# Kernel optimization log

Hardware: AMD Instinct MI355X
Metric: run time of the kernel (lower is better)

## Reference

```python
import jax, jax.numpy as jnp
import numpy as np
from jax import lax

EPS = 1e-5


def fps(xyz, npoint):
    # Farthest point sampling; xyz [B, N, 3] -> idx [B, npoint] (starts at point 0)
    B, N, _ = xyz.shape

    def body(carry, _):
        dist, far = carry
        c = jnp.take_along_axis(xyz, far[:, None, None], axis=1)  # [B,1,3]
        d = jnp.sum((xyz - c) ** 2, -1)                            # [B,N]
        dist = jnp.minimum(dist, d)
        nxt = jnp.argmax(dist, -1).astype(jnp.int32)
        return (dist, nxt), far

    init = (jnp.full((B, N), 1e10, xyz.dtype), jnp.zeros((B,), jnp.int32))
    _, idx = lax.scan(body, init, None, length=npoint)
    return idx.T  # [B, npoint]


def query_ball(radius, nsample, xyz, new_xyz):
    # xyz [B,N,3], new_xyz [B,S,3] -> idx [B,S,nsample]
    N = xyz.shape[1]
    sqr = jnp.sum((new_xyz[:, :, None, :] - xyz[:, None, :, :]) ** 2, -1)  # [B,S,N]
    idx = jnp.where(sqr > radius * radius, N, jnp.arange(N)[None, None, :])
    idx = jnp.sort(idx, axis=-1)[:, :, :nsample]
    # out-of-ball slots get replaced by the first in-ball index (torch repo behavior)
    return jnp.where(idx == N, idx[:, :, :1], idx)


def gather_pts(x, idx):
    # x [B,N,C], idx [B,...] -> [B,...,C]
    B = x.shape[0]
    b = jnp.arange(B).reshape((B,) + (1,) * (idx.ndim - 1))
    return x[b, idx]


def mlp_bn(x, layers):
    # x [B,S,K,C]; shared 1x1-conv MLP + training-mode BatchNorm + ReLU
    for w, g, b in layers:
        x = jnp.einsum('bskc,oc->bsko', x, w)
        mean = x.mean((0, 1, 2))
        var = x.var((0, 1, 2))  # biased, as torch BN uses for normalization
        x = jax.nn.relu((x - mean) * lax.rsqrt(var + EPS) * g + b)
    return x


def set_abstraction(xyz, points, npoint, radius, nsample, layers, group_all):
    B = xyz.shape[0]
    if group_all:
        new_xyz = jnp.zeros((B, 1, 3), xyz.dtype)
        new_points = xyz[:, None]  # [B,1,N,3] (raw xyz, no centering)
        if points is not None:
            new_points = jnp.concatenate([new_points, points[:, None]], -1)
    else:
        fidx = fps(xyz, npoint)
        new_xyz = gather_pts(xyz, fidx)                     # [B,S,3]
        idx = query_ball(radius, nsample, xyz, new_xyz)     # [B,S,K]
        grouped = gather_pts(xyz, idx) - new_xyz[:, :, None, :]
        if points is not None:
            new_points = jnp.concatenate([grouped, gather_pts(points, idx)], -1)
        else:
            new_points = grouped
    feat = mlp_bn(new_points, layers).max(2)  # max-pool over neighbors -> [B,S,C]
    return new_xyz, feat


def _forward(xyz_time, l1, l2, l3):
    B, T, N, _ = xyz_time.shape
    x = xyz_time.reshape(B * T, N, 4)
    xyz, t = x[..., :3], x[..., 3:]
    x1_xyz, x1 = set_abstraction(xyz, t, 512, 0.2, 32, l1, False)
    x2_xyz, x2 = set_abstraction(x1_xyz, x1, 128, 0.4, 64, l2, False)
    _, x3 = set_abstraction(x2_xyz, x2, None, None, None, l3, True)
    return x3.reshape(B, T, -1)


def setup_inputs() -> dict:
    key = jax.random.key(0)
    ks = jax.random.split(key, 16)
    inp = {"xyz_time": jax.random.uniform(ks[0], (2, 4, 4096, 4), jnp.float32)}
    specs = {1: [(64, 4), (64, 64), (128, 64)],
             2: [(128, 131), (128, 128), (256, 128)],
             3: [(256, 259), (512, 256), (1024, 512)]}
    i = 1
    for s, layers in specs.items():
        for j, (o, c) in enumerate(layers):
            inp[f"w{s}_{j}"] = jax.random.normal(jax.random.fold_in(ks[i], j), (o, c), jnp.float32) * 0.1
            inp[f"g{s}_{j}"] = jnp.ones((o,), jnp.float32)
            inp[f"b{s}_{j}"] = jnp.zeros((o,), jnp.float32)
        i += 1
    return inp


def reference(xyz_time, w1_0, g1_0, b1_0, w1_1, g1_1, b1_1, w1_2, g1_2, b1_2,
              w2_0, g2_0, b2_0, w2_1, g2_1, b2_1, w2_2, g2_2, b2_2,
              w3_0, g3_0, b3_0, w3_1, g3_1, b3_1, w3_2, g3_2, b3_2):
    l1 = [(w1_0, g1_0, b1_0), (w1_1, g1_1, b1_1), (w1_2, g1_2, b1_2)]
    l2 = [(w2_0, g2_0, b2_0), (w2_1, g2_1, b2_1), (w2_2, g2_2, b2_2)]
    l3 = [(w3_0, g3_0, b3_0), (w3_1, g3_1, b3_1), (w3_2, g3_2, b3_2)]
    return _forward(xyz_time, l1, l2, l3)
```

## Files before the change

### kernel.cpp

```cpp
#include <hip/hip_runtime.h>


typedef short s16x8 __attribute__((ext_vector_type(8)));
typedef float f32x4 __attribute__((ext_vector_type(4)));

__device__ __forceinline__ unsigned short f2bf_rne(float f) {
    unsigned u = __float_as_uint(f);
    u += 0x7FFFu + ((u >> 16) & 1u);
    return (unsigned short)(u >> 16);
}
__device__ __forceinline__ void f2bf_split(float v, unsigned short& hi,
                                           unsigned short& lo) {
    unsigned u = __float_as_uint(v);
    unsigned r = u + 0x7FFFu + ((u >> 16) & 1u);
    hi = (unsigned short)(r >> 16);
    float vh = __uint_as_float(r & 0xFFFF0000u);
    lo = f2bf_rne(v - vh);
}

__device__ __forceinline__ unsigned long long umax64(unsigned long long a,
                                                     unsigned long long b) {
    return a > b ? a : b;
}

__device__ __forceinline__ unsigned wred_umax63(unsigned v) {
    unsigned t;
    t = (unsigned)__builtin_amdgcn_update_dpp(0, (int)v, 0x111, 0xf, 0xf, true); if (t > v) v = t;
    t = (unsigned)__builtin_amdgcn_update_dpp(0, (int)v, 0x112, 0xf, 0xf, true); if (t > v) v = t;
    t = (unsigned)__builtin_amdgcn_update_dpp(0, (int)v, 0x114, 0xf, 0xf, true); if (t > v) v = t;
    t = (unsigned)__builtin_amdgcn_update_dpp(0, (int)v, 0x118, 0xf, 0xf, true); if (t > v) v = t;
    t = (unsigned)__builtin_amdgcn_update_dpp(0, (int)v, 0x142, 0xa, 0xf, true); if (t > v) v = t;
    t = (unsigned)__builtin_amdgcn_update_dpp(0, (int)v, 0x143, 0xc, 0xf, true); if (t > v) v = t;
    return v;
}

__device__ __forceinline__ void wave_argmax(unsigned dbits, unsigned nInv,
                                            unsigned& vmax, unsigned& iInv) {
    unsigned m = wred_umax63(dbits);
    vmax = (unsigned)__builtin_amdgcn_readlane((int)m, 63);
    unsigned cand = (dbits == vmax) ? nInv : 0u;
    unsigned im = wred_umax63(cand);
    iInv = (unsigned)__builtin_amdgcn_readlane((int)im, 63);
}

struct PWArgs {
    const float* w[9];
    unsigned off[9];
    int O[9], C[9], CP[9];
};
__device__ __forceinline__ void prep_w_dev(const PWArgs& a,
                                           unsigned short* __restrict__ wh,
                                           unsigned short* __restrict__ wl,
                                           int i) {
    int l = 0;
#pragma unroll
    for (int k = 1; k < 9; ++k) if (i >= (int)a.off[k]) l = k;
    int li = i - (int)a.off[l];
    int CP = a.CP[l];
    int o = li / CP;
    int c = li - o * CP;
    float v = (c < a.C[l]) ? a.w[l][(size_t)o * a.C[l] + c] : 0.f;
    unsigned short h, lo;
    f2bf_split(v, h, lo);
    wh[i] = h; wl[i] = lo;
}

template<int NT, int ITEMS, int STRIDE>
__global__ __launch_bounds__(NT) void fps_block(
    const float* __restrict__ pts, int npoint,
    int* __restrict__ outIdx, float* __restrict__ outXyz,
    int nFps, PWArgs pw, unsigned short* __restrict__ wh,
    unsigned short* __restrict__ wl, int wtotal)
{
    constexpr int N = NT * ITEMS;
    constexpr int NW = NT / 64;
    __shared__ float4 scoord[N];
    __shared__ unsigned long long wkey[2][NW];

    if (blockIdx.x >= nFps) {
        int i = (blockIdx.x - nFps) * NT + threadIdx.x;
        if (i < wtotal) prep_w_dev(pw, wh, wl, i);
        return;
    }

    const int b = blockIdx.x;
    const int tid = threadIdx.x;
    const int wid = tid >> 6;
    const int lane = tid & 63;
    const float* P = pts + (size_t)b * N * STRIDE;

    float px[ITEMS], py[ITEMS], pz[ITEMS], dloc[ITEMS];
#pragma unroll
    for (int w = 0; w < ITEMS; ++w) {
        int n = tid + w * NT;
        float x, y, z;
        if (STRIDE == 4) {
            float4 v = *(const float4*)(P + (size_t)n * 4);
            x = v.x; y = v.y; z = v.z;
        } else {
            x = P[(size_t)n * STRIDE + 0];
            y = P[(size_t)n * STRIDE + 1];
            z = P[(size_t)n * STRIDE + 2];
        }
        px[w] = x; py[w] = y; pz[w] = z;
        scoord[n] = make_float4(x, y, z, 0.f);
        dloc[w] = 1e10f;
    }
    __syncthreads();
    float4 c0 = scoord[0];
    float cx = c0.x, cy = c0.y, cz = c0.z;
    int far = 0;

    for (int i = 0; i < npoint; ++i) {
        if (tid == 0) {
            outIdx[(size_t)b * npoint + i] = far;
            outXyz[((size_t)b * npoint + i) * 3 + 0] = cx;
            outXyz[((size_t)b * npoint + i) * 3 + 1] = cy;
            outXyz[((size_t)b * npoint + i) * 3 + 2] = cz;
        }
        float bestV = -1.0f;
        int bestW = 0;
#pragma unroll
        for (int w = 0; w < ITEMS; ++w) {
            float dx = __fsub_rn(px[w], cx);
            float dy = __fsub_rn(py[w], cy);
            float dz = __fsub_rn(pz[w], cz);
            float d = __fadd_rn(__fadd_rn(__fmul_rn(dx, dx), __fmul_rn(dy, dy)),
                                __fmul_rn(dz, dz));
            float dd = fminf(dloc[w], d);
            dloc[w] = dd;
            if (dd > bestV) { bestV = dd; bestW = w; }
        }
        int bestN = tid + bestW * NT;
        unsigned vmax, iInv;
        wave_argmax(__float_as_uint(bestV), 0xFFFFFFFFu ^ (unsigned)bestN,
                    vmax, iInv);
        const int par = i & 1;
        if (lane == 0)
            wkey[par][wid] = ((unsigned long long)vmax << 32) | iInv;
        __syncthreads();
        unsigned long long kb = wkey[par][0];
#pragma unroll
        for (int w2 = 1; w2 < NW; ++w2) kb = umax64(kb, wkey[par][w2]);
        far = (int)(0xFFFFFFFFu ^ (unsigned)kb);
        float4 cc = scoord[far];
        cx = cc.x; cy = cc.y; cz = cc.z;
    }
}

__device__ void fps_wave_dev(const float* __restrict__ pts, int npoint,
                             int* __restrict__ outIdx, float* __restrict__ outXyz,
                             int b, float4* scoord)
{
    constexpr int ITEMS = 8;
    constexpr int STRIDE = 3;
    constexpr int N = 64 * ITEMS;
    const int tid = threadIdx.x;
    const float* P = pts + (size_t)b * N * STRIDE;

    float px[ITEMS], py[ITEMS], pz[ITEMS], dloc[ITEMS];
#pragma unroll
    for (int w = 0; w < ITEMS; ++w) {
        int n = tid + w * 64;
        float x = P[(size_t)n * STRIDE + 0];
        float y = P[(size_t)n * STRIDE + 1];
        float z = P[(size_t)n * STRIDE + 2];
        px[w] = x; py[w] = y; pz[w] = z;
        scoord[n] = make_float4(x, y, z, 0.f);
        dloc[w] = 1e10f;
    }
    __threadfence_block();
    float4 c0 = scoord[0];
    float cx = c0.x, cy = c0.y, cz = c0.z;
    int far = 0;

    for (int i = 0; i < npoint; ++i) {
        if (tid == 0) {
            outIdx[(size_t)b * npoint + i] = far;
            outXyz[((size_t)b * npoint + i) * 3 + 0] = cx;
            outXyz[((size_t)b * npoint + i) * 3 + 1] = cy;
            outXyz[((size_t)b * npoint + i) * 3 + 2] = cz;
        }
        float bestV = -1.0f;
        int bestW = 0;
#pragma unroll
        for (int w = 0; w < ITEMS; ++w) {
            float dx = __fsub_rn(px[w], cx);
            float dy = __fsub_rn(py[w], cy);
            float dz = __fsub_rn(pz[w], cz);
            float d = __fadd_rn(__fadd_rn(__fmul_rn(dx, dx), __fmul_rn(dy, dy)),
                                __fmul_rn(dz, dz));
            float dd = fminf(dloc[w], d);
            dloc[w] = dd;
            if (dd > bestV) { bestV = dd; bestW = w; }
        }
        int bestN = tid + bestW * 64;
        unsigned vmax, iInv;
        wave_argmax(__float_as_uint(bestV), 0xFFFFFFFFu ^ (unsigned)bestN,
                    vmax, iInv);
        far = (int)(0xFFFFFFFFu ^ iInv);
        float4 cc = scoord[far];
        cx = cc.x; cy = cc.y; cz = cc.z;
    }
}

__global__ __launch_bounds__(256) void qb_group1(
    const float* __restrict__ xyz ,
    const float* __restrict__ ctr ,
    const float* __restrict__ W0 ,
    float* __restrict__ Yout ,
    double* __restrict__ pS0, double* __restrict__ pQ0,
    int nQb, const float* __restrict__ fpsPts,
    int* __restrict__ fpsIdx, float* __restrict__ fpsXyz)
{
    __shared__ float4 scoord[512];
    __shared__ float4 srows[4][32];
    __shared__ float sstat[4][64][2];
    if ((int)blockIdx.x >= nQb) {
        if (threadIdx.x < 64)
            fps_wave_dev(fpsPts, 128, fpsIdx, fpsXyz,
                         (int)blockIdx.x - nQb, scoord);
        return;
    }
    const int tid = threadIdx.x;
    const int gw = (blockIdx.x * 256 + tid) >> 6;
    const int wid = tid >> 6;
    const int lane = tid & 63;
    int b = gw >> 9;
    const float* P = xyz + (size_t)b * 4096 * 4;
    float cx = ctr[(size_t)gw * 3 + 0];
    float cy = ctr[(size_t)gw * 3 + 1];
    float cz = ctr[(size_t)gw * 3 + 2];
    int cnt = 0;
    float f0x = 0.f, f0y = 0.f, f0z = 0.f, f0t = 0.f;
    bool haveFirst = false;
    for (int base = 0; base < 4096 && cnt < 32; base += 64) {
        int n = base + lane;
        float4 p = *(const float4*)(P + (size_t)n * 4);
        float ex = __fsub_rn(p.x, cx);
        float ey = __fsub_rn(p.y, cy);
        float ez = __fsub_rn(p.z, cz);
        float d = __fadd_rn(__fadd_rn(__fmul_rn(ex, ex), __fmul_rn(ey, ey)),
                            __fmul_rn(ez, ez));
        bool inb = !(d > 0.04f);
        unsigned long long mask = __ballot(inb);
        if (mask) {
            if (!haveFirst) {
                int fl = (int)__builtin_ctzll(mask);
                f0x = __shfl(ex, fl); f0y = __shfl(ey, fl);
                f0z = __shfl(ez, fl); f0t = __shfl(p.w, fl);
                haveFirst = true;
            }
            if (inb) {
                int pos = cnt + __builtin_popcountll(mask & ((1ull << lane) - 1ull));
                if (pos < 32)
                    srows[wid][pos] = make_float4(ex, ey, ez, p.w);
            }
            cnt += (int)__builtin_popcountll(mask);
        }
    }
    if (cnt > 32) cnt = 32;
    for (int p2 = cnt + lane; p2 < 32; p2 += 64)
        srows[wid][p2] = make_float4(f0x, f0y, f0z, f0t);
    __syncthreads();

    float wc0 = W0[lane * 4 + 0];
    float wc1 = W0[lane * 4 + 1];
    float wc2 = W0[lane * 4 + 2];
    float wc3 = W0[lane * 4 + 3];
    float s = 0.f, s2 = 0.f;
    float* yp = Yout + (size_t)gw * 32 * 64 + lane;
#pragma unroll 4
    for (int r = 0; r < 32; ++r) {
        float4 e = srows[wid][r];
        float y = e.x * wc0 + e.y * wc1 + e.z * wc2 + e.w * wc3;
        yp[(size_t)r * 64] = y;
        s += y;
        s2 += y * y;
    }
    sstat[wid][lane][0] = s;
    sstat[wid][lane][1] = s2;
    __syncthreads();
    if (tid < 64) {
        double S = 0.0, S2 = 0.0;
#pragma unroll
        for (int w2 = 0; w2 < 4; ++w2) {
            S += (double)sstat[w2][tid][0];
            S2 += (double)sstat[w2][tid][1];
        }
        atomicAdd(&pS0[tid], S);
        atomicAdd(&pQ0[tid], S2);
    }
}

__device__ __forceinline__ void qb2_dev(
    const float* __restrict__ xyz, const float* __restrict__ centers,
    int* __restrict__ outIdx, int gw, int lane)
{
    const int N = 512, stride = 3, S = 128, nsample = 64;
    const float r2 = 0.16f;
    int b = gw / S;
    const float* P = xyz + (size_t)b * N * stride;
    float cx = centers[(size_t)gw * 3 + 0];
    float cy = centers[(size_t)gw * 3 + 1];
    float cz = centers[(size_t)gw * 3 + 2];
    int* out = outIdx + (size_t)gw * nsample;
    int cnt = 0;
    int firstIdx = 0;
    bool haveFirst = false;
    for (int base = 0; base < N && cnt < nsample; base += 64) {
        int n = base + lane;
        bool inb = false;
        if (n < N) {
            float dx = __fsub_rn(cx, P[(size_t)n * stride + 0]);
            float dy = __fsub_rn(cy, P[(size_t)n * stride + 1]);
            float dz = __fsub_rn(cz, P[(size_t)n * stride + 2]);
            float d = __fadd_rn(__fadd_rn(__fmul_rn(dx, dx), __fmul_rn(dy, dy)),
                                __fmul_rn(dz, dz));
            inb = !(d > r2);
        }
        unsigned long long mask = __ballot(inb);
        if (mask) {
            if (!haveFirst) { firstIdx = base + __builtin_ctzll(mask); haveFirst = true; }
            if (inb) {
                int pos = cnt + __builtin_popcountll(mask & ((1ull << lane) - 1ull));
                if (pos < nsample) out[pos] = n;
            }
            cnt += (int)__builtin_popcountll(mask);
        }
    }
    if (cnt > nsample) cnt = nsample;
    for (int p = cnt + lane; p < nsample; p += 64) out[p] = firstIdx;
}

__global__ __launch_bounds__(256) void gemm_fused(
    const float* __restrict__ X,
    const double* __restrict__ pSin, const double* __restrict__ pQin,
    const float* __restrict__ gIn, const float* __restrict__ bIn,
    double invMin, int applyAct,
    const unsigned short* __restrict__ Bh, const unsigned short* __restrict__ Bl,
    float* __restrict__ Y,
    double* __restrict__ pSout, double* __restrict__ pQout,
    int AC, int CPW, int O, int gmode,
    const int* __restrict__ gqb, const float* __restrict__ gxyz,
    const float* __restrict__ gctr, const float* __restrict__ gfeat,
    int redK, float* __restrict__ Vmax, float* __restrict__ Vmin)
{
    constexpr int PITCH = 40;
    __shared__ __align__(16) unsigned short sAh[128 * PITCH];
    __shared__ __align__(16) unsigned short sAl[128 * PITCH];
    __shared__ __align__(16) unsigned short sBh[128 * PITCH];
    __shared__ __align__(16) unsigned short sBl[128 * PITCH];
    __shared__ float sred[2048];
    __shared__ float sScale[512];
    __shared__ float sShift[512];

    const int tid = threadIdx.x;
    const int lane = tid & 63;
    const int wid = tid >> 6;
    const int col15 = lane & 15;
    const int quad = lane >> 4;
    const int wm = (wid >> 1) * 64;
    const int wo = (wid & 1) * 64;
    const int m0 = blockIdx.x * 128;
    const int o0 = blockIdx.y * 128;
    const int lr = tid >> 2;
    const int lc = (tid & 3) * 8;

    if (applyAct) {
        for (int c = tid; c < AC; c += 256) {
            double S = pSin[c], Q = pQin[c];
            double mean = S * invMin;
            double var = Q * invMin - mean * mean;
            float varf = (float)var;
            if (varf < 0.f) varf = 0.f;
            float sc = gIn[c] * rsqrtf(varf + 1e-5f);
            sScale[c] = sc;
            sShift[c] = bIn[c] - (float)mean * sc;
        }
    }
    __syncthreads();

    f32x4 acc[4][4];
#pragma unroll
    for (int mt = 0; mt < 4; ++mt)
#pragma unroll
        for (int ot = 0; ot < 4; ++ot)
            acc[mt][ot] = {0.f, 0.f, 0.f, 0.f};

    for (int k0 = 0; k0 < CPW; k0 += 32) {
#pragma unroll
        for (int it = 0; it < 2; ++it) {
            int r = lr + it * 64;
            int c = k0 + lc;
            unsigned short h[8], l[8];
            float vv[8];
            bool have = true;
            if (gmode == 0) {
                if (c + 8 <= AC) {
                    const float* xr = X + (size_t)(m0 + r) * AC + c;
                    float4 v0 = *(const float4*)xr;
                    float4 v1 = *(const float4*)(xr + 4);
                    vv[0] = v0.x; vv[1] = v0.y; vv[2] = v0.z; vv[3] = v0.w;
                    vv[4] = v1.x; vv[5] = v1.y; vv[6] = v1.z; vv[7] = v1.w;
                    if (applyAct) {
#pragma unroll
                        for (int j = 0; j < 8; ++j)
                            vv[j] = fmaxf(vv[j] * sScale[c + j] + sShift[c + j], 0.f);
                    }
                } else {
                    have = false;
                }
            } else if (gmode == 2) {
                int m = m0 + r;
                int idx = gqb[m];
                idx = (idx < 0) ? 0 : (idx > 511 ? 511 : idx);
                int bb2 = m >> 13;
                int bs = m >> 6;
                const float* frow = gfeat + ((size_t)bb2 * 512 + idx) * 128;
                const float* xrow = gxyz + ((size_t)bb2 * 512 + idx) * 3;
                const float* crow = gctr + (size_t)bs * 3;
#pragma unroll
                for (int j = 0; j < 8; ++j) {
                    int cc = c + j;
                    float v = 0.f;
                    if (cc < 3)        v = __fsub_rn(xrow[cc], crow[cc]);
                    else if (cc < 131) v = frow[cc - 3];
                    vv[j] = v;
                }
            } else {
                int m = m0 + r;
                const float* frow = gfeat + (size_t)m * 256;
                const float* crow = gctr + (size_t)m * 3;
#pragma unroll
                for (int j = 0; j < 8; ++j) {
                    int cc = c + j;
                    float v = 0.f;
                    if (cc < 3)        v = crow[cc];
                    else if (cc < 259) v = frow[cc - 3];
                    vv[j] = v;
                }
            }
            if (have) {
#pragma unroll
                for (int j = 0; j < 8; ++j) f2bf_split(vv[j], h[j], l[j]);
            } else {
#pragma unroll
                for (int j = 0; j < 8; ++j) { h[j] = 0; l[j] = 0; }
            }
            *(ushort4*)&sAh[r * PITCH + lc] = make_ushort4(h[0], h[1], h[2], h[3]);
            *(ushort4*)&sAh[r * PITCH + lc + 4] = make_ushort4(h[4], h[5], h[6], h[7]);
            *(ushort4*)&sAl[r * PITCH + lc] = make_ushort4(l[0], l[1], l[2], l[3]);
            *(ushort4*)&sAl[r * PITCH + lc + 4] = make_ushort4(l[4], l[5], l[6], l[7]);
        }
#pragma unroll
        for (int it = 0; it < 2; ++it) {
            int r = lr + it * 64;
            int c = k0 + lc;
            int o = o0 + r;
            uint4 vh = {0, 0, 0, 0}, vl = {0, 0, 0, 0};
            if (o < O && c < CPW) {
                size_t goff = (size_t)o * CPW + c;
                vh = *(const uint4*)(Bh + goff);
                vl = *(const uint4*)(Bl + goff);
            }
            *(uint4*)&sBh[r * PITCH + lc] = vh;
            *(uint4*)&sBl[r * PITCH + lc] = vl;
        }
        __syncthreads();
        s16x8 ah[4], al[4], bh[4], bl[4];
#pragma unroll
        for (int mt = 0; mt < 4; ++mt) {
            int rowoff = (wm + mt * 16 + col15) * PITCH + quad * 8;
            ah[mt] = *(const s16x8*)&sAh[rowoff];
            al[mt] = *(const s16x8*)&sAl[rowoff];
        }
#pragma unroll
        for (int ot = 0; ot < 4; ++ot) {
            int rowoff = (wo + ot * 16 + col15) * PITCH + quad * 8;
            bh[ot] = *(const s16x8*)&sBh[rowoff];
            bl[ot] = *(const s16x8*)&sBl[rowoff];
        }
#pragma unroll
        for (int mt = 0; mt < 4; ++mt)
#pragma unroll
            for (int ot = 0; ot < 4; ++ot) {
                acc[mt][ot] = __builtin_amdgcn_mfma_f32_16x16x32_bf16(
                    ah[mt], bl[ot], acc[mt][ot], 0, 0, 0);
                acc[mt][ot] = __builtin_amdgcn_mfma_f32_16x16x32_bf16(
                    al[mt], bh[ot], acc[mt][ot], 0, 0, 0);
                acc[mt][ot] = __builtin_amdgcn_mfma_f32_16x16x32_bf16(
                    ah[mt], bh[ot], acc[mt][ot], 0, 0, 0);
            }
        __syncthreads();
    }
    if (redK == 0) {
#pragma unroll
        for (int mt = 0; mt < 4; ++mt)
#pragma unroll
            for (int ot = 0; ot < 4; ++ot) {
                int og = o0 + wo + ot * 16 + col15;
                if (og < O) {
#pragma unroll
                    for (int r = 0; r < 4; ++r) {
                        int mg = m0 + wm + mt * 16 + quad * 4 + r;
                        Y[(size_t)mg * O + og] = acc[mt][ot][r];
                    }
                }
            }
    } else if (redK == 32) {
#pragma unroll
        for (int ot = 0; ot < 4; ++ot) {
            int og = o0 + wo + ot * 16 + col15;
#pragma unroll
            for (int cp = 0; cp < 2; ++cp) {
                float mx = acc[2 * cp][ot][0];
                float mn = mx;
#pragma unroll
                for (int mi = 0; mi < 2; ++mi)
#pragma unroll
                    for (int r = 0; r < 4; ++r) {
                        float v = acc[2 * cp + mi][ot][r];
                        mx = fmaxf(mx, v);
                        mn = fminf(mn, v);
                    }
                mx = fmaxf(mx, __shfl_xor(mx, 16));
                mx = fmaxf(mx, __shfl_xor(mx, 32));
                mn = fminf(mn, __shfl_xor(mn, 16));
                mn = fminf(mn, __shfl_xor(mn, 32));
                if (quad == 0) {
                    int ctr = (m0 >> 5) + (wm >> 5) + cp;
                    Vmax[(size_t)ctr * O + og] = mx;
                    Vmin[(size_t)ctr * O + og] = mn;
                }
            }
        }
    } else {
#pragma unroll
        for (int ot = 0; ot < 4; ++ot) {
            int og = o0 + wo + ot * 16 + col15;
            float mx = acc[0][ot][0];
            float mn = mx;
#pragma unroll
            for (int mt = 0; mt < 4; ++mt)
#pragma unroll
                for (int r = 0; r < 4; ++r) {
                    float v = acc[mt][ot][r];
                    mx = fmaxf(mx, v);
                    mn = fminf(mn, v);
                }
            mx = fmaxf(mx, __shfl_xor(mx, 16));
            mx = fmaxf(mx, __shfl_xor(mx, 32));
            mn = fminf(mn, __shfl_xor(mn, 16));
            mn = fminf(mn, __shfl_xor(mn, 32));
            if (quad == 0) {
                int ctr = (m0 >> 6) + (wm >> 6);
                Vmax[(size_t)ctr * O + og] = mx;
                Vmin[(size_t)ctr * O + og] = mn;
            }
        }
    }
#pragma unroll
    for (int ot = 0; ot < 4; ++ot) {
        float s = 0.f, s2 = 0.f;
#pragma unroll
        for (int mt = 0; mt < 4; ++mt)
#pragma unroll
            for (int r = 0; r < 4; ++r) {
                float v = acc[mt][ot][r];
                s += v;
                s2 += v * v;
            }
        int slot = ((wid * 4 + quad) * 16 + col15) * 4 + ot;
        sred[slot * 2] = s;
        sred[slot * 2 + 1] = s2;
    }
    __syncthreads();
    if (tid < 128) {
        int col = tid;
        int o = o0 + col;
        if (o < O) {
            int cb = col >> 6;
            int ot = (col & 63) >> 4;
            int c15 = col & 15;
            double S = 0.0, S2 = 0.0;
#pragma unroll
            for (int wp = 0; wp < 2; ++wp) {
                int wd = cb + wp * 2;
#pragma unroll
                for (int q = 0; q < 4; ++q) {
                    int slot = ((wd * 4 + q) * 16 + c15) * 4 + ot;
                    S += (double)sred[slot * 2];
                    S2 += (double)sred[slot * 2 + 1];
                }
            }
            atomicAdd(&pSout[o], S);
            atomicAdd(&pQout[o], S2);
        }
    }
}

__global__ __launch_bounds__(256) void bn_relu_max(
    const float* __restrict__ Y, const float* __restrict__ Vmin,
    const double* __restrict__ pS, const double* __restrict__ pQ,
    const float* __restrict__ gv, const float* __restrict__ bv, double invM,
    float* __restrict__ out, int Stot, int K, int O, int vmode, int nMain,
    const float* __restrict__ qbXyz, const float* __restrict__ qbCtr,
    int* __restrict__ qbOut)
{
    if ((int)blockIdx.x >= nMain) {
        int wid = threadIdx.x >> 6, lane = threadIdx.x & 63;
        int gw = ((int)blockIdx.x - nMain) * 4 + wid;
        if (gw < 1024) qb2_dev(qbXyz, qbCtr, qbOut, gw, lane);
        return;
    }
    int idx = blockIdx.x * 256 + threadIdx.x;
    if (idx >= Stot * O) return;
    int s = idx / O;
    int o = idx - s * O;
    double S = pS[o], Q = pQ[o];
    double mean = S * invM;
    double var = Q * invM - mean * mean;
    float varf = (float)var;
    if (varf < 0.f) varf = 0.f;
    float sc = gv[o] * rsqrtf(varf + 1e-5f);
    float sh = bv[o] - (float)mean * sc;
    if (vmode) {
        float vmax = Y[(size_t)s * O + o];
        float vmin = Vmin[(size_t)s * O + o];
        float v = (sc >= 0.f) ? vmax : vmin;
        out[idx] = fmaxf(v * sc + sh, 0.f);
        return;
    }
    const float* basep = Y + (size_t)s * K * O + o;
    float mx = 0.f;
    for (int k = 0; k < K; ++k) {
        float v = basep[(size_t)k * O] * sc + sh;
        v = fmaxf(v, 0.f);
        mx = fmaxf(mx, v);
    }
    out[idx] = mx;
}

extern "C" void kernel_launch(void* const* d_in, const int* in_sizes, int n_in,
                              void* d_out, int out_size, void* d_ws, size_t ws_size,
                              hipStream_t stream)
{
    const float* xin = (const float*)d_in[0];
    const float* w[9]; const float* g[9]; const float* bb[9];
    for (int i = 0; i < 9; ++i) {
        w[i]  = (const float*)d_in[1 + 3 * i];
        g[i]  = (const float*)d_in[2 + 3 * i];
        bb[i] = (const float*)d_in[3 + 3 * i];
    }

    char* base = (char*)d_ws;
    size_t off = 0;
    auto alloc = [&](size_t bytes) -> void* {
        void* p = base + off;
        off = (off + bytes + 255) & ~(size_t)255;
        return p;
    };
    const int OC[9][3] = {{64,4,8},{64,64,64},{128,64,64},
                          {128,131,136},{128,128,128},{256,128,128},
                          {256,259,264},{512,256,256},{1024,512,512}};
    size_t woff[10]; woff[0] = 0;
    for (int i = 0; i < 9; ++i) woff[i + 1] = woff[i] + (size_t)OC[i][0] * OC[i][2];

    int*    fps1   = (int*)alloc((size_t)4096 * 4);
    int*    fps2   = (int*)alloc((size_t)1024 * 4);
    int*    qb2    = (int*)alloc((size_t)65536 * 4);
    float*  nx1    = (float*)alloc((size_t)12288 * 4);
    float*  nx2    = (float*)alloc((size_t)3072 * 4);
    float*  feat1  = (float*)alloc((size_t)524288 * 4);
    float*  feat2  = (float*)alloc((size_t)262144 * 4);
    double* partS  = (double*)alloc((size_t)9 * 1024 * 8);
    double* partQ  = (double*)alloc((size_t)9 * 1024 * 8);
    unsigned short* WH = (unsigned short*)alloc(woff[9] * 2);
    unsigned short* WL = (unsigned short*)alloc(woff[9] * 2);
    const size_t zeroBytes = off;
    float*  XG = (float*)alloc((size_t)65536 * 136 * 4);
    float*  A  = (float*)alloc((size_t)16777216 * 4);
    if (off > ws_size) return;

    hipMemsetAsync(d_ws, 0, zeroBytes, stream);

    PWArgs pwa;
    for (int i = 0; i < 9; ++i) {
        pwa.w[i] = w[i]; pwa.off[i] = (unsigned)woff[i];
        pwa.O[i] = OC[i][0]; pwa.C[i] = OC[i][1]; pwa.CP[i] = OC[i][2];
    }
    const int nPrep = (int)((woff[9] + 255) / 256);

    auto gemm = [&](const float* X, int prevLi, double invMprev, int li,
                    float* Y, int YB, int OB, int AC, int CPW, int O,
                    int gmode, const int* gqb, const float* gxyz,
                    const float* gctr, const float* gfeat,
                    int redK, float* Vmax, float* Vmin) {
        gemm_fused<<<dim3(YB, OB), 256, 0, stream>>>(
            X,
            prevLi >= 0 ? partS + (size_t)prevLi * 1024 : nullptr,
            prevLi >= 0 ? partQ + (size_t)prevLi * 1024 : nullptr,
            prevLi >= 0 ? g[prevLi] : nullptr,
            prevLi >= 0 ? bb[prevLi] : nullptr,
            invMprev, prevLi >= 0 ? 1 : 0,
            WH + woff[li], WL + woff[li], Y,
            partS + (size_t)li * 1024, partQ + (size_t)li * 1024,
            AC, CPW, O, gmode, gqb, gxyz, gctr, gfeat, redK, Vmax, Vmin);
    };

    const double inv1 = 1.0 / 131072.0;
    const double inv2 = 1.0 / 65536.0;
    const double inv3 = 1.0 / 1024.0;

    fps_block<256, 16, 4><<<8 + nPrep, 256, 0, stream>>>(
        xin, 512, fps1, nx1, 8, pwa, WH, WL, (int)woff[9]);
    qb_group1<<<1024 + 8, 256, 0, stream>>>(
        xin, nx1, w[0], A, partS + 0, partQ + 0, 1024, nx1, fps2, nx2);

    gemm(A, 0, inv1, 1, XG, 1024, 1, 64, 64, 64, 0, nullptr, nullptr, nullptr, nullptr, 0, nullptr, nullptr);
    gemm(XG, 1, inv1, 2, A, 1024, 1, 64, 64, 128, 0, nullptr, nullptr, nullptr, nullptr, 32, A, A + 524288);
    bn_relu_max<<<2048 + 256, 256, 0, stream>>>(
        A, A + 524288, partS + 2 * 1024, partQ + 2 * 1024, g[2], bb[2], inv1,
        feat1, 4096, 32, 128, 1, 2048, nx1, nx2, qb2);

    gemm(nullptr, -1, 0.0, 3, XG, 512, 1, 136, 136, 128, 2, qb2, nx1, nx2, feat1, 0, nullptr, nullptr);
    gemm(XG, 3, inv2, 4, A, 512, 1, 128, 128, 128, 0, nullptr, nullptr, nullptr, nullptr, 0, nullptr, nullptr);
    gemm(A, 4, inv2, 5, XG, 512, 2, 128, 128, 256, 0, nullptr, nullptr, nullptr, nullptr, 64, XG, XG + 262144);
    bn_relu_max<<<(1024 * 256) / 256, 256, 0, stream>>>(
        XG, XG + 262144, partS + 5 * 1024, partQ + 5 * 1024, g[5], bb[5], inv2,
        feat2, 1024, 64, 256, 1, 1024 * 256 / 256, nullptr, nullptr, nullptr);

    gemm(nullptr, -1, 0.0, 6, A, 8, 2, 264, 264, 256, 3, nullptr, nullptr, nx2, feat2, 0, nullptr, nullptr);
    gemm(A, 6, inv3, 7, XG, 8, 4, 256, 256, 512, 0, nullptr, nullptr, nullptr, nullptr, 0, nullptr, nullptr);
    gemm(XG, 7, inv3, 8, A, 8, 8, 512, 512, 1024, 0, nullptr, nullptr, nullptr, nullptr, 0, nullptr, nullptr);
    bn_relu_max<<<(8 * 1024) / 256, 256, 0, stream>>>(
        A, nullptr, partS + 8 * 1024, partQ + 8 * 1024, g[8], bb[8], inv3,
        (float*)d_out, 8, 128, 1024, 0, (8 * 1024) / 256,
        nullptr, nullptr, nullptr);
}
```

Before: 767.0 us.

## Fuse BN-ReLU-max finalize into next GEMM's gather and move ball query

Removes the two intermediate bn_relu_max launches for SA1 and SA2. The next GEMM's gather stage now picks the stored max or min value according to the BN scale sign, then applies BN and ReLU inline. The second ball-query work, which previously rode on the removed bn_relu_max launch, is appended as extra blocks to the first layer-1 GEMM launch. This cuts two kernel launches and the feat1/feat2 buffers, at the cost of repeating the BN transform per gathered element, since grouped rows are re-read many times.

```diff
diff --git a/kernel.cpp b/kernel.cpp
--- a/kernel.cpp
+++ b/kernel.cpp
@@ -337,14 +337,17 @@
     const float* __restrict__ X,
     const double* __restrict__ pSin, const double* __restrict__ pQin,
     const float* __restrict__ gIn, const float* __restrict__ bIn,
-    double invMin, int applyAct,
+    double invMin, int actMode, int bnCh,
     const unsigned short* __restrict__ Bh, const unsigned short* __restrict__ Bl,
     float* __restrict__ Y,
     double* __restrict__ pSout, double* __restrict__ pQout,
     int AC, int CPW, int O, int gmode,
     const int* __restrict__ gqb, const float* __restrict__ gxyz,
     const float* __restrict__ gctr, const float* __restrict__ gfeat,
-    int redK, float* __restrict__ Vmax, float* __restrict__ Vmin)
+    const float* __restrict__ gfmin,
+    int redK, float* __restrict__ Vmax, float* __restrict__ Vmin,
+    int nMain, const float* __restrict__ qbXyz,
+    const float* __restrict__ qbCtr, int* __restrict__ qbOut)
 {
     constexpr int PITCH = 40;
     __shared__ __align__(16) unsigned short sAh[128 * PITCH];
@@ -354,6 +357,13 @@
     __shared__ float sred[2048];
     __shared__ float sScale[512];
     __shared__ float sShift[512];
+
+    if ((int)blockIdx.x >= nMain) {
+        int wid = threadIdx.x >> 6, lane = threadIdx.x & 63;
+        int gw = ((int)blockIdx.x - nMain) * 4 + wid;
+        if (gw < 1024) qb2_dev(qbXyz, qbCtr, qbOut, gw, lane);
+        return;
+    }
 
     const int tid = threadIdx.x;
     const int lane = tid & 63;
@@ -367,8 +377,8 @@
     const int lr = tid >> 2;
     const int lc = (tid & 3) * 8;
 
-    if (applyAct) {
-        for (int c = tid; c < AC; c += 256) {
+    if (bnCh > 0) {
+        for (int c = tid; c < bnCh; c += 256) {
             double S = pSin[c], Q = pQin[c];
             double mean = S * invMin;
             double var = Q * invMin - mean * mean;
@@ -403,7 +413,7 @@
                     float4 v1 = *(const float4*)(xr + 4);
                     vv[0] = v0.x; vv[1] = v0.y; vv[2] = v0.z; vv[3] = v0.w;
                     vv[4] = v1.x; vv[5] = v1.y; vv[6] = v1.z; vv[7] = v1.w;
-                    if (applyAct) {
+                    if (actMode == 1) {
 #pragma unroll
                         for (int j = 0; j < 8; ++j)
                             vv[j] = fmaxf(vv[j] * sScale[c + j] + sShift[c + j], 0.f);
@@ -417,27 +427,40 @@
                 idx = (idx < 0) ? 0 : (idx > 511 ? 511 : idx);
                 int bb2 = m >> 13;
                 int bs = m >> 6;
-                const float* frow = gfeat + ((size_t)bb2 * 512 + idx) * 128;
-                const float* xrow = gxyz + ((size_t)bb2 * 512 + idx) * 3;
+                int ctrg = bb2 * 512 + idx;
+                const float* fmx = gfeat + (size_t)ctrg * 128;
+                const float* fmn = gfmin + (size_t)ctrg * 128;
+                const float* xrow = gxyz + (size_t)ctrg * 3;
                 const float* crow = gctr + (size_t)bs * 3;
 #pragma unroll
                 for (int j = 0; j < 8; ++j) {
                     int cc = c + j;
                     float v = 0.f;
                     if (cc < 3)        v = __fsub_rn(xrow[cc], crow[cc]);
-                    else if (cc < 131) v = frow[cc - 3];
+                    else if (cc < 131) {
+                        int fc = cc - 3;
+                        float sc = sScale[fc];
+                        float sel = (sc >= 0.f) ? fmx[fc] : fmn[fc];
+                        v = fmaxf(sel * sc + sShift[fc], 0.f);
+                    }
                     vv[j] = v;
                 }
             } else {
                 int m = m0 + r;
-                const float* frow = gfeat + (size_t)m * 256;
+                const float* fmx = gfeat + (size_t)m * 256;
+                const float* fmn = gfmin + (size_t)m * 256;
                 const float* crow = gctr + (size_t)m * 3;
 #pragma unroll
                 for (int j = 0; j < 8; ++j) {
                     int cc = c + j;
                     float v = 0.f;
                     if (cc < 3)        v = crow[cc];
-                    else if (cc < 259) v = frow[cc - 3];
+                    else if (cc < 259) {
+                        int fc = cc - 3;
+                        float sc = sScale[fc];
+                        float sel = (sc >= 0.f) ? fmx[fc] : fmn[fc];
+                        v = fmaxf(sel * sc + sShift[fc], 0.f);
+                    }
                     vv[j] = v;
                 }
             }
@@ -601,19 +624,11 @@
 }
 
 __global__ __launch_bounds__(256) void bn_relu_max(
-    const float* __restrict__ Y, const float* __restrict__ Vmin,
+    const float* __restrict__ Y,
     const double* __restrict__ pS, const double* __restrict__ pQ,
     const float* __restrict__ gv, const float* __restrict__ bv, double invM,
-    float* __restrict__ out, int Stot, int K, int O, int vmode, int nMain,
-    const float* __restrict__ qbXyz, const float* __restrict__ qbCtr,
-    int* __restrict__ qbOut)
+    float* __restrict__ out, int Stot, int K, int O)
 {
-    if ((int)blockIdx.x >= nMain) {
-        int wid = threadIdx.x >> 6, lane = threadIdx.x & 63;
-        int gw = ((int)blockIdx.x - nMain) * 4 + wid;
-        if (gw < 1024) qb2_dev(qbXyz, qbCtr, qbOut, gw, lane);
-        return;
-    }
     int idx = blockIdx.x * 256 + threadIdx.x;
     if (idx >= Stot * O) return;
     int s = idx / O;
@@ -625,13 +640,6 @@
     if (varf < 0.f) varf = 0.f;
     float sc = gv[o] * rsqrtf(varf + 1e-5f);
     float sh = bv[o] - (float)mean * sc;
-    if (vmode) {
-        float vmax = Y[(size_t)s * O + o];
-        float vmin = Vmin[(size_t)s * O + o];
-        float v = (sc >= 0.f) ? vmax : vmin;
-        out[idx] = fmaxf(v * sc + sh, 0.f);
-        return;
-    }
     const float* basep = Y + (size_t)s * K * O + o;
     float mx = 0.f;
     for (int k = 0; k < K; ++k) {
@@ -672,8 +680,6 @@
     int*    qb2    = (int*)alloc((size_t)65536 * 4);
     float*  nx1    = (float*)alloc((size_t)12288 * 4);
     float*  nx2    = (float*)alloc((size_t)3072 * 4);
-    float*  feat1  = (float*)alloc((size_t)524288 * 4);
-    float*  feat2  = (float*)alloc((size_t)262144 * 4);
     double* partS  = (double*)alloc((size_t)9 * 1024 * 8);
     double* partQ  = (double*)alloc((size_t)9 * 1024 * 8);
     unsigned short* WH = (unsigned short*)alloc(woff[9] * 2);
@@ -692,21 +698,23 @@
     }
     const int nPrep = (int)((woff[9] + 255) / 256);
 
-    auto gemm = [&](const float* X, int prevLi, double invMprev, int li,
-                    float* Y, int YB, int OB, int AC, int CPW, int O,
-                    int gmode, const int* gqb, const float* gxyz,
-                    const float* gctr, const float* gfeat,
-                    int redK, float* Vmax, float* Vmin) {
-        gemm_fused<<<dim3(YB, OB), 256, 0, stream>>>(
+    auto gemm = [&](const float* X, int prevLi, double invMprev, int actMode,
+                    int bnCh, int li, float* Y, int YB, int OB, int AC,
+                    int CPW, int O, int gmode, const int* gqb,
+                    const float* gxyz, const float* gctr, const float* gfeat,
+                    const float* gfmin, int redK, float* Vmax, float* Vmin,
+                    int extraQB, const float* qx, const float* qc, int* qo) {
+        gemm_fused<<<dim3(YB + extraQB, OB), 256, 0, stream>>>(
             X,
             prevLi >= 0 ? partS + (size_t)prevLi * 1024 : nullptr,
             prevLi >= 0 ? partQ + (size_t)prevLi * 1024 : nullptr,
             prevLi >= 0 ? g[prevLi] : nullptr,
             prevLi >= 0 ? bb[prevLi] : nullptr,
-            invMprev, prevLi >= 0 ? 1 : 0,
+            invMprev, actMode, bnCh,
             WH + woff[li], WL + woff[li], Y,
             partS + (size_t)li * 1024, partQ + (size_t)li * 1024,
-            AC, CPW, O, gmode, gqb, gxyz, gctr, gfeat, redK, Vmax, Vmin);
+            AC, CPW, O, gmode, gqb, gxyz, gctr, gfeat, gfmin,
+            redK, Vmax, Vmin, YB, qx, qc, qo);
     };
 
     const double inv1 = 1.0 / 131072.0;
@@ -718,24 +726,33 @@
     qb_group1<<<1024 + 8, 256, 0, stream>>>(
         xin, nx1, w[0], A, partS + 0, partQ + 0, 1024, nx1, fps2, nx2);
 
-    gemm(A, 0, inv1, 1, XG, 1024, 1, 64, 64, 64, 0, nullptr, nullptr, nullptr, nullptr, 0, nullptr, nullptr);
-    gemm(XG, 1, inv1, 2, A, 1024, 1, 64, 64, 128, 0, nullptr, nullptr, nullptr, nullptr, 32, A, A + 524288);
-    bn_relu_max<<<2048 + 256, 256, 0, stream>>>(
-        A, A + 524288, partS + 2 * 1024, partQ + 2 * 1024, g[2], bb[2], inv1,
-        feat1, 4096, 32, 128, 1, 2048, nx1, nx2, qb2);
-
-    gemm(nullptr, -1, 0.0, 3, XG, 512, 1, 136, 136, 128, 2, qb2, nx1, nx2, feat1, 0, nullptr, nullptr);
-    gemm(XG, 3, inv2, 4, A, 512, 1, 128, 128, 128, 0, nullptr, nullptr, nullptr, nullptr, 0, nullptr, nullptr);
-    gemm(A, 4, inv2, 5, XG, 512, 2, 128, 128, 256, 0, nullptr, nullptr, nullptr, nullptr, 64, XG, XG + 262144);
-    bn_relu_max<<<(1024 * 256) / 256, 256, 0, stream>>>(
-        XG, XG + 262144, partS + 5 * 1024, partQ + 5 * 1024, g[5], bb[5], inv2,
-        feat2, 1024, 64, 256, 1, 1024 * 256 / 256, nullptr, nullptr, nullptr);
-
-    gemm(nullptr, -1, 0.0, 6, A, 8, 2, 264, 264, 256, 3, nullptr, nullptr, nx2, feat2, 0, nullptr, nullptr);
-    gemm(A, 6, inv3, 7, XG, 8, 4, 256, 256, 512, 0, nullptr, nullptr, nullptr, nullptr, 0, nullptr, nullptr);
-    gemm(XG, 7, inv3, 8, A, 8, 8, 512, 512, 1024, 0, nullptr, nullptr, nullptr, nullptr, 0, nullptr, nullptr);
+    gemm(A, 0, inv1, 1, 64, 1, XG, 1024, 1, 64, 64, 64, 0,
+         nullptr, nullptr, nullptr, nullptr, nullptr, 0, nullptr, nullptr,
+         256, nx1, nx2, qb2);
+    gemm(XG, 1, inv1, 1, 64, 2, A, 1024, 1, 64, 64, 128, 0,
+         nullptr, nullptr, nullptr, nullptr, nullptr, 32, A, A + 524288,
+         0, nullptr, nullptr, nullptr);
+
+    gemm(nullptr, 2, inv1, 2, 128, 3, XG, 512, 1, 136, 136, 128, 2,
+         qb2, nx1, nx2, A, A + 524288, 0, nullptr, nullptr,
+         0, nullptr, nullptr, nullptr);
+    gemm(XG, 3, inv2, 1, 128, 4, A, 512, 1, 128, 128, 128, 0,
+         nullptr, nullptr, nullptr, nullptr, nullptr, 0, nullptr, nullptr,
+         0, nullptr, nullptr, nullptr);
+    gemm(A, 4, inv2, 1, 128, 5, XG, 512, 2, 128, 128, 256, 0,
+         nullptr, nullptr, nullptr, nullptr, nullptr, 64, XG, XG + 262144,
+         0, nullptr, nullptr, nullptr);
+
+    gemm(nullptr, 5, inv2, 2, 256, 6, A, 8, 2, 264, 264, 256, 3,
+         nullptr, nullptr, nx2, XG, XG + 262144, 0, nullptr, nullptr,
+         0, nullptr, nullptr, nullptr);
+    gemm(A, 6, inv3, 1, 256, 7, XG, 8, 4, 256, 256, 512, 0,
+         nullptr, nullptr, nullptr, nullptr, nullptr, 0, nullptr, nullptr,
+         0, nullptr, nullptr, nullptr);
+    gemm(XG, 7, inv3, 1, 512, 8, A, 8, 8, 512, 512, 1024, 0,
+         nullptr, nullptr, nullptr, nullptr, nullptr, 0, nullptr, nullptr,
+         0, nullptr, nullptr, nullptr);
     bn_relu_max<<<(8 * 1024) / 256, 256, 0, stream>>>(
-        A, nullptr, partS + 8 * 1024, partQ + 8 * 1024, g[8], bb[8], inv3,
-        (float*)d_out, 8, 128, 1024, 0, (8 * 1024) / 256,
-        nullptr, nullptr, nullptr);
-}
+        A, partS + 8 * 1024, partQ + 8 * 1024, g[8], bb[8], inv3,
+        (float*)d_out, 8, 128, 1024);
+}
```

After: 774.7 us. No clear change (+1.0%).
